# Optimization experiments

Hardware: AMD Instinct MI355X
Metric: run time of the kernel (lower is better)

Reference implementation:

```python
import jax, jax.numpy as jnp
import numpy as np

B, T, D, H = 4, 1024, 1024, 16


def setup_inputs() -> dict:
    key = jax.random.key(0)
    ks = jax.random.split(key, 7)
    x = jax.random.normal(ks[0], (B, T, D), dtype=jnp.float32)
    scale = 0.02
    Wq = jax.random.normal(ks[1], (D, D), dtype=jnp.float32) * scale
    Wk = jax.random.normal(ks[2], (D, D), dtype=jnp.float32) * scale
    Wv = jax.random.normal(ks[3], (D, D), dtype=jnp.float32) * scale
    bq = jax.random.normal(ks[4], (D,), dtype=jnp.float32) * scale
    bk = jax.random.normal(ks[5], (D,), dtype=jnp.float32) * scale
    bv = jax.random.normal(ks[6], (D,), dtype=jnp.float32) * scale
    temperature = jnp.ones((H, 1, 1), dtype=jnp.float32)  # nn.Parameter(torch.ones(H,1,1))
    return {"x": x, "Wq": Wq, "bq": bq, "Wk": Wk, "bk": bk, "Wv": Wv, "bv": bv,
            "temperature": temperature}


def reference(x, Wq, bq, Wk, bk, Wv, bv, temperature):
    b, t, d = x.shape
    h = temperature.shape[0]
    dh = d // h
    # torch: self.q(x).view(B, H, -1, T)  -- a RAW reshape of (B,T,D) -> (B,H,Dh,T)
    q = (x @ Wq + bq).reshape(b, h, dh, t)
    k = (x @ Wk + bk).reshape(b, h, dh, t)
    v = (x @ Wv + bv).reshape(b, h, dh, t)
    # attn = k^T @ v : (B,H,T,T), scaled per-head by temperature, softmax over last dim
    attn = jnp.einsum('bhdt,bhds->bhts', k, v) * temperature
    attn = jax.nn.softmax(attn, axis=-1)
    # out = q @ attn : (B,H,Dh,T), then RAW reshape back to (B,T,D)
    out = jnp.einsum('bhdt,bhts->bhds', q, attn)
    return out.reshape(b, t, d)
```

## Files before the change

### kernel.cpp

```cpp
#include <hip/hip_runtime.h>
#include <math.h>

#define Bv 4
#define Tv 1024
#define Dv 1024
#define Hv 16
#define DHv 64

typedef __attribute__((ext_vector_type(8))) short short8;
typedef __attribute__((ext_vector_type(4))) short short4v;
typedef __attribute__((ext_vector_type(4))) float f32x4;

#define MFMA16(a, b, c) __builtin_amdgcn_mfma_f32_16x16x32_bf16((a), (b), (c), 0, 0, 0)

__device__ __forceinline__ short f2bf(float f) {
    union { float f; unsigned u; } v; v.f = f;
    unsigned r = v.u + 0x7FFFu + ((v.u >> 16) & 1u);
    return (short)(r >> 16);
}

__device__ __forceinline__ void async16(const void* g, void* l) {
    __builtin_amdgcn_global_load_lds(
        (const __attribute__((address_space(1))) void*)g,
        (__attribute__((address_space(3))) void*)l, 16, 0, 0);
}

__device__ __forceinline__ short8 frag64(const short* buf, int r, int cw) {
    return *(const short8*)&buf[r * 64 + ((cw ^ (r & 7)) << 3)];
}

__device__ __forceinline__ short8 frag32(const short* buf, int r, int cw) {
    return *(const short8*)&buf[r * 32 + (((cw ^ r) & 3) << 3)];
}

__global__ __launch_bounds__(256) void cast_x(const float* __restrict__ x, short* __restrict__ xb) {
    const int idx = blockIdx.x * 256 + threadIdx.x;
    float4 v = ((const float4*)x)[idx];
    short4v o;
    o[0] = f2bf(v.x); o[1] = f2bf(v.y); o[2] = f2bf(v.z); o[3] = f2bf(v.w);
    ((short4v*)xb)[idx] = o;
}

__global__ __launch_bounds__(256) void w_cast_t(
    const float* __restrict__ Wq, const float* __restrict__ Wk, const float* __restrict__ Wv,
    short* __restrict__ Wt)
{
    const float* W = (blockIdx.z == 0) ? Wq : (blockIdx.z == 1) ? Wk : Wv;
    short* Wto = Wt + (size_t)blockIdx.z * 1048576;
    __shared__ short Tl[64 * 72];
    const int k0 = blockIdx.y * 64, n0 = blockIdx.x * 64;
    const int tid = threadIdx.x;
    {
        const int r = tid >> 2, c16 = (tid & 3) * 16;
        const float* src = W + (size_t)(k0 + r) * Dv + n0 + c16;
        float4 f0 = ((const float4*)src)[0], f1 = ((const float4*)src)[1];
        float4 f2 = ((const float4*)src)[2], f3 = ((const float4*)src)[3];
        short8 s0, s1;
        s0[0] = f2bf(f0.x); s0[1] = f2bf(f0.y); s0[2] = f2bf(f0.z); s0[3] = f2bf(f0.w);
        s0[4] = f2bf(f1.x); s0[5] = f2bf(f1.y); s0[6] = f2bf(f1.z); s0[7] = f2bf(f1.w);
        s1[0] = f2bf(f2.x); s1[1] = f2bf(f2.y); s1[2] = f2bf(f2.z); s1[3] = f2bf(f2.w);
        s1[4] = f2bf(f3.x); s1[5] = f2bf(f3.y); s1[6] = f2bf(f3.z); s1[7] = f2bf(f3.w);
        *(short8*)&Tl[r * 72 + c16] = s0;
        *(short8*)&Tl[r * 72 + c16 + 8] = s1;
    }
    __syncthreads();
#pragma unroll
    for (int p = 0; p < 2; p++) {
        const int n = p * 32 + (tid >> 3), j8 = (tid & 7) * 8;
        short8 o;
#pragma unroll
        for (int jj = 0; jj < 8; jj++) o[jj] = Tl[(j8 + jj) * 72 + n];
        *(short8*)&Wto[(size_t)(n0 + n) * Dv + k0 + j8] = o;
    }
}

__device__ __forceinline__ void stage_tile(
    const short* __restrict__ xb, const short* __restrict__ Wt,
    const int* aOff, const int* bOff, const int* dOff,
    short* smem, int sl, int k)
{
#pragma unroll
    for (int p = 0; p < 2; p++) {
        async16(xb + aOff[p] + k, smem + sl + dOff[p]);
        async16(Wt + bOff[p] + k, smem + 24576 + sl + dOff[p]);
    }
}

__device__ __forceinline__ void compute_tile(
    const short* smem, int sl, int RM, int CN, int c, int q, f32x4 acc[8][4])
{
    const short* Ac = smem + sl;
    const short* Bc = smem + 24576 + sl;
    short8 bf[4], af[8];
#pragma unroll
    for (int j = 0; j < 4; j++) bf[j] = frag32(Bc, CN + j * 16 + c, q);
#pragma unroll
    for (int m = 0; m < 8; m++) af[m] = frag32(Ac, RM + m * 16 + c, q);
    __builtin_amdgcn_s_setprio(1);
#pragma unroll
    for (int m = 0; m < 8; m++)
#pragma unroll
        for (int j = 0; j < 4; j++)
            acc[m][j] = MFMA16(af[m], bf[j], acc[m][j]);
    __builtin_amdgcn_s_setprio(0);
}

__global__ __launch_bounds__(512, 2) void qkv_mfma(
    const short* __restrict__ xb, const short* __restrict__ Wt3,
    const float* __restrict__ bq, const float* __restrict__ bk, const float* __restrict__ bv,
    short* __restrict__ Qo, short* __restrict__ Kt, short* __restrict__ Vt)
{
    const int z = blockIdx.z;
    const short* Wt = Wt3 + (size_t)z * 1048576;
    const float* bias = (z == 0) ? bq : (z == 1) ? bk : bv;

    __shared__ short smem[49152];

    const int tid = threadIdx.x;
    const int lane = tid & 63, w = tid >> 6;
    const int q = lane >> 4, c = lane & 15;
    const int wr = w >> 2, wc = w & 3;
    const int RM = wr * 128, CN = wc * 64;
    const int bm = blockIdx.y * 256, bn = blockIdx.x * 256;

    int aOff[2], bOff[2], dOff[2];
#pragma unroll
    for (int p = 0; p < 2; p++) {
        const int idx = p * 512 + tid;
        const int r = idx >> 2, cs = idx & 3, cg = (cs ^ r) & 3;
        aOff[p] = (bm + r) * Dv + cg * 8;
        bOff[p] = (bn + r) * Dv + cg * 8;
        dOff[p] = idx * 8;
    }

    f32x4 acc[8][4] = {};

    stage_tile(xb, Wt, aOff, bOff, dOff, smem, 0, 0);
    stage_tile(xb, Wt, aOff, bOff, dOff, smem, 8192, 32);

    int slC = 0, slS = 16384;
#pragma unroll 1
    for (int i = 0; i < 30; i++) {
        asm volatile("s_waitcnt vmcnt(4)" ::: "memory");
        __builtin_amdgcn_s_barrier();
        __builtin_amdgcn_sched_barrier(0);
        stage_tile(xb, Wt, aOff, bOff, dOff, smem, slS, (i + 2) * 32);
        compute_tile(smem, slC, RM, CN, c, q, acc);
        slC += 8192; if (slC == 24576) slC = 0;
        slS += 8192; if (slS == 24576) slS = 0;
    }
    asm volatile("s_waitcnt vmcnt(4)" ::: "memory");
    __builtin_amdgcn_s_barrier();
    __builtin_amdgcn_sched_barrier(0);
    compute_tile(smem, slC, RM, CN, c, q, acc);
    slC += 8192; if (slC == 24576) slC = 0;
    asm volatile("s_waitcnt vmcnt(0)" ::: "memory");
    __builtin_amdgcn_s_barrier();
    __builtin_amdgcn_sched_barrier(0);
    compute_tile(smem, slC, RM, CN, c, q, acc);

    if (z == 0) {
#pragma unroll
        for (int j = 0; j < 4; j++) {
            const int col = bn + CN + j * 16 + c;
            const float bb = bias[col];
#pragma unroll
            for (int m = 0; m < 8; m++) {
#pragma unroll
                for (int r = 0; r < 4; r++) {
                    const int row = bm + RM + m * 16 + q * 4 + r;
                    Qo[(size_t)row * Dv + col] = f2bf(acc[m][j][r] + bb);
                }
            }
        }
    } else {
        short* dst = (z == 1) ? Kt : Vt;
        short* T = smem;
        const int hb = bm >> 6;
#pragma unroll
        for (int nh = 0; nh < 2; nh++) {
            __syncthreads();
            if ((wc >> 1) == nh) {
#pragma unroll
                for (int j = 0; j < 4; j++) {
                    const int nl = (wc & 1) * 64 + j * 16 + c;
                    const float bb = bias[bn + nh * 128 + nl];
#pragma unroll
                    for (int m = 0; m < 8; m++) {
                        short4v pk;
#pragma unroll
                        for (int r = 0; r < 4; r++) pk[r] = f2bf(acc[m][j][r] + bb);
                        *(short4v*)&T[nl * 264 + RM + m * 16 + q * 4] = pk;
                    }
                }
            }
            __syncthreads();
#pragma unroll
            for (int p = 0; p < 8; p++) {
                const int idx = p * 512 + tid;
                const int n = idx >> 5, k2 = idx & 31;
                short8 v = *(const short8*)&T[n * 264 + k2 * 8];
                const size_t addr = (size_t)(hb + (k2 >> 3)) * 65536 +
                                    (size_t)(bn + nh * 128 + n) * 64 + (k2 & 7) * 8;
                *(short8*)&dst[addr] = v;
            }
        }
    }
}

__global__ __launch_bounds__(256) void attn_stats(
    const short* __restrict__ Kt, const short* __restrict__ Vt,
    const float* __restrict__ temp,
    float* __restrict__ mOut, float* __restrict__ zOut)
{
    const int b = blockIdx.z, h = blockIdx.y, t0 = blockIdx.x * 64;
    const int bh = b * Hv + h;
    const float ts = temp[h];
    __shared__ short Ks[64 * 64];
    __shared__ short Vs[128 * 64];
    const int tid = threadIdx.x;
    const int lane = tid & 63, w = tid >> 6;
    const int q = lane >> 4, c = lane & 15;
    const short* Kbase = Kt + (size_t)bh * 65536;
    const short* Vbase = Vt + (size_t)bh * 65536;

#pragma unroll
    for (int p = 0; p < 2; p++) {
        const int idx = p * 256 + tid;
        const int r = idx >> 3, cs = idx & 7, cg = cs ^ (r & 7);
        async16(Kbase + (size_t)(t0 + r) * 64 + cg * 8, Ks + idx * 8);
    }

    float m_run[4], z_run[4];
#pragma unroll
    for (int r = 0; r < 4; r++) { m_run[r] = -INFINITY; z_run[r] = 0.f; }

    short8 aK0, aK1;
    for (int s0 = 0; s0 < Tv; s0 += 128) {
        __syncthreads();
#pragma unroll
        for (int p = 0; p < 4; p++) {
            const int idx = p * 256 + tid;
            const int r = idx >> 3, cs = idx & 7, cg = cs ^ (r & 7);
            async16(Vbase + (size_t)(s0 + r) * 64 + cg * 8, Vs + idx * 8);
        }
        __syncthreads();
        if (s0 == 0) {
            aK0 = frag64(Ks, w * 16 + c, q);
            aK1 = frag64(Ks, w * 16 + c, 4 + q);
        }
        float lv[8][4];
#pragma unroll
        for (int sf = 0; sf < 8; sf++) {
            short8 b0 = frag64(Vs, sf * 16 + c, q);
            short8 b1 = frag64(Vs, sf * 16 + c, 4 + q);
            f32x4 l = {0.f, 0.f, 0.f, 0.f};
            l = MFMA16(aK0, b0, l);
            l = MFMA16(aK1, b1, l);
#pragma unroll
            for (int r = 0; r < 4; r++) lv[sf][r] = l[r] * ts;
        }
#pragma unroll
        for (int r = 0; r < 4; r++) {
            float vmax = lv[0][r];
#pragma unroll
            for (int sf = 1; sf < 8; sf++) vmax = fmaxf(vmax, lv[sf][r]);
            float mn = fmaxf(m_run[r], vmax);
            float za = 0.f;
#pragma unroll
            for (int sf = 0; sf < 8; sf++) za += __expf(lv[sf][r] - mn);
            z_run[r] = z_run[r] * __expf(m_run[r] - mn) + za;
            m_run[r] = mn;
        }
    }
#pragma unroll
    for (int mask = 1; mask <= 8; mask <<= 1) {
#pragma unroll
        for (int r = 0; r < 4; r++) {
            float om = __shfl_xor(m_run[r], mask, 64);
            float oz = __shfl_xor(z_run[r], mask, 64);
            float mn = fmaxf(m_run[r], om);
            z_run[r] = z_run[r] * __expf(m_run[r] - mn) + oz * __expf(om - mn);
            m_run[r] = mn;
        }
    }
    if (c == 0) {
#pragma unroll
        for (int r = 0; r < 4; r++) {
            const int t = t0 + w * 16 + q * 4 + r;
            mOut[(size_t)bh * Tv + t] = m_run[r];
            zOut[(size_t)bh * Tv + t] = 1.f / z_run[r];
        }
    }
}

__global__ __launch_bounds__(256) void attn_out(
    const short* __restrict__ Qb, const short* __restrict__ Kt, const short* __restrict__ Vt,
    const float* __restrict__ temp, const float* __restrict__ mIn, const float* __restrict__ zIn,
    float* __restrict__ out)
{
    const int b = blockIdx.z, h = blockIdx.y, s0 = blockIdx.x * 128;
    const int bh = b * Hv + h;
    const float ts = temp[h];
    __shared__ short Vs[128 * 64];
    __shared__ short Ks[64 * 64];
    __shared__ short Qs[64 * 64];
    __shared__ short Pt[128 * 72];
    __shared__ float ms[64], zs[64];
    const int tid = threadIdx.x;
    const int lane = tid & 63, w = tid >> 6;
    const int q = lane >> 4, c = lane & 15;
    const short* Vbase = Vt + (size_t)bh * 65536;
    const short* Kbase = Kt + (size_t)bh * 65536;
    const short* Qbase = Qb + (size_t)(b * Tv + h * DHv) * Dv;

#pragma unroll
    for (int p = 0; p < 4; p++) {
        const int idx = p * 256 + tid;
        const int r = idx >> 3, cs = idx & 7, cg = cs ^ (r & 7);
        async16(Vbase + (size_t)(s0 + r) * 64 + cg * 8, Vs + idx * 8);
    }

    f32x4 acc[8] = {};

    for (int t0 = 0; t0 < Tv; t0 += 64) {
        __syncthreads();
#pragma unroll
        for (int p = 0; p < 2; p++) {
            const int idx = p * 256 + tid;
            const int r = idx >> 3, cs = idx & 7, cg = cs ^ (r & 7);
            async16(Kbase + (size_t)(t0 + r) * 64 + cg * 8, Ks + idx * 8);
            async16(Qbase + (size_t)r * Dv + t0 + cg * 8, Qs + idx * 8);
        }
        if (tid < 64) {
            ms[tid] = mIn[(size_t)bh * Tv + t0 + tid];
            zs[tid] = zIn[(size_t)bh * Tv + t0 + tid];
        }
        __syncthreads();

        short8 aK0 = frag64(Ks, w * 16 + c, q);
        short8 aK1 = frag64(Ks, w * 16 + c, 4 + q);
#pragma unroll
        for (int sf = 0; sf < 8; sf++) {
            short8 b0 = frag64(Vs, sf * 16 + c, q);
            short8 b1 = frag64(Vs, sf * 16 + c, 4 + q);
            f32x4 l = {0.f, 0.f, 0.f, 0.f};
            l = MFMA16(aK0, b0, l);
            l = MFMA16(aK1, b1, l);
            short4v p4;
#pragma unroll
            for (int r = 0; r < 4; r++) {
                const int tr = w * 16 + q * 4 + r;
                float p = __expf(l[r] * ts - ms[tr]) * zs[tr];
                p4[r] = f2bf(p);
            }
            *(short4v*)&Pt[(sf * 16 + c) * 72 + w * 16 + q * 4] = p4;
        }
        __syncthreads();

        short8 aQ0 = frag64(Qs, w * 16 + c, q);
        short8 aQ1 = frag64(Qs, w * 16 + c, 4 + q);
#pragma unroll
        for (int sf = 0; sf < 8; sf++) {
            short8 p0 = *(const short8*)&Pt[(sf * 16 + c) * 72 + q * 8];
            short8 p1 = *(const short8*)&Pt[(sf * 16 + c) * 72 + 32 + q * 8];
            acc[sf] = MFMA16(aQ0, p0, acc[sf]);
            acc[sf] = MFMA16(aQ1, p1, acc[sf]);
        }
    }

#pragma unroll
    for (int sf = 0; sf < 8; sf++) {
#pragma unroll
        for (int r = 0; r < 4; r++) {
            const int d = w * 16 + q * 4 + r;
            out[(size_t)(b * Tv + h * DHv + d) * Dv + s0 + sf * 16 + c] = acc[sf][r];
        }
    }
}

extern "C" void kernel_launch(void* const* d_in, const int* in_sizes, int n_in,
                              void* d_out, int out_size, void* d_ws, size_t ws_size,
                              hipStream_t stream) {
    const float* x    = (const float*)d_in[0];
    const float* Wq   = (const float*)d_in[1];
    const float* bq   = (const float*)d_in[2];
    const float* Wk   = (const float*)d_in[3];
    const float* bk   = (const float*)d_in[4];
    const float* Wv   = (const float*)d_in[5];
    const float* bv   = (const float*)d_in[6];
    const float* temp = (const float*)d_in[7];
    float* out = (float*)d_out;

    char* ws = (char*)d_ws;
    short* xb = (short*)(ws);
    short* Wt = (short*)(ws + ((size_t)8 << 20));
    short* Qb = (short*)(ws + ((size_t)14 << 20));
    short* Kt = (short*)(ws + ((size_t)22 << 20));
    short* Vt = (short*)(ws + ((size_t)30 << 20));
    float* mbuf = (float*)(ws + ((size_t)38 << 20));
    float* zbuf = mbuf + 65536;

    cast_x<<<4096, 256, 0, stream>>>(x, xb);
    w_cast_t<<<dim3(16, 16, 3), 256, 0, stream>>>(Wq, Wk, Wv, Wt);
    qkv_mfma<<<dim3(4, 16, 3), 512, 0, stream>>>(xb, Wt, bq, bk, bv, Qb, Kt, Vt);
    attn_stats<<<dim3(16, 16, 4), 256, 0, stream>>>(Kt, Vt, temp, mbuf, zbuf);
    attn_out<<<dim3(8, 16, 4), 256, 0, stream>>>(Qb, Kt, Vt, temp, mbuf, zbuf, out);
}
```

Baseline: 188.0 us.

## Double-buffer K/Q and V tiles in attention kernels, keep V fragments in registers

Both attention kernels now prefetch the next K/Q or V tile into a second LDS buffer while the current tile is computed. This removes one barrier per iteration and hides global load latency. attn_out holds the V fragments in registers, reuses the V region for the swizzled P tile, and loads all m/z statistics up front with async copies. Blocks are remapped so neighbouring workgroups share bh, and launch bounds plus s_setprio are added around the MFMA sections. The extra registers and LDS may lower occupancy, and the manual lgkmcnt barrier has to be ordered correctly.

```diff
diff --git a/kernel.cpp b/kernel.cpp
--- a/kernel.cpp
+++ b/kernel.cpp
@@ -31,6 +31,13 @@
 
 __device__ __forceinline__ short8 frag32(const short* buf, int r, int cw) {
     return *(const short8*)&buf[r * 32 + (((cw ^ r) & 3) << 3)];
+}
+
+__device__ __forceinline__ void lds_barrier() {
+    asm volatile("s_waitcnt lgkmcnt(0)" ::: "memory");
+    __builtin_amdgcn_sched_barrier(0);
+    __builtin_amdgcn_s_barrier();
+    __builtin_amdgcn_sched_barrier(0);
 }
 
 __global__ __launch_bounds__(256) void cast_x(const float* __restrict__ x, short* __restrict__ xb) {
@@ -208,58 +215,71 @@
     }
 }
 
-__global__ __launch_bounds__(256) void attn_stats(
+__global__ __launch_bounds__(256, 4) void attn_stats(
     const short* __restrict__ Kt, const short* __restrict__ Vt,
     const float* __restrict__ temp,
     float* __restrict__ mOut, float* __restrict__ zOut)
 {
-    const int b = blockIdx.z, h = blockIdx.y, t0 = blockIdx.x * 64;
-    const int bh = b * Hv + h;
-    const float ts = temp[h];
+    const int L = blockIdx.x + 16 * (blockIdx.y + 16 * blockIdx.z);
+    const int bh = (L & 7) + 8 * (L >> 7);
+    const int t0 = ((L >> 3) & 15) * 64;
+    const float ts = temp[bh & 15];
     __shared__ short Ks[64 * 64];
-    __shared__ short Vs[128 * 64];
+    __shared__ short Vs[2][128 * 64];
     const int tid = threadIdx.x;
     const int lane = tid & 63, w = tid >> 6;
     const int q = lane >> 4, c = lane & 15;
     const short* Kbase = Kt + (size_t)bh * 65536;
     const short* Vbase = Vt + (size_t)bh * 65536;
 
+    int vOff[4], vDst[4];
+#pragma unroll
+    for (int p = 0; p < 4; p++) {
+        const int idx = p * 256 + tid;
+        const int r = idx >> 3, cs = idx & 7, cg = cs ^ (r & 7);
+        vOff[p] = r * 64 + cg * 8;
+        vDst[p] = idx * 8;
+    }
 #pragma unroll
     for (int p = 0; p < 2; p++) {
         const int idx = p * 256 + tid;
         const int r = idx >> 3, cs = idx & 7, cg = cs ^ (r & 7);
         async16(Kbase + (size_t)(t0 + r) * 64 + cg * 8, Ks + idx * 8);
     }
+#pragma unroll
+    for (int p = 0; p < 4; p++) async16(Vbase + vOff[p], &Vs[0][0] + vDst[p]);
 
     float m_run[4], z_run[4];
 #pragma unroll
     for (int r = 0; r < 4; r++) { m_run[r] = -INFINITY; z_run[r] = 0.f; }
 
     short8 aK0, aK1;
-    for (int s0 = 0; s0 < Tv; s0 += 128) {
+#pragma unroll 1
+    for (int i = 0; i < 8; i++) {
         __syncthreads();
-#pragma unroll
-        for (int p = 0; p < 4; p++) {
-            const int idx = p * 256 + tid;
-            const int r = idx >> 3, cs = idx & 7, cg = cs ^ (r & 7);
-            async16(Vbase + (size_t)(s0 + r) * 64 + cg * 8, Vs + idx * 8);
-        }
-        __syncthreads();
-        if (s0 == 0) {
+        if (i < 7) {
+            const short* src = Vbase + (i + 1) * 8192;
+#pragma unroll
+            for (int p = 0; p < 4; p++) async16(src + vOff[p], &Vs[(i + 1) & 1][0] + vDst[p]);
+        }
+        if (i == 0) {
             aK0 = frag64(Ks, w * 16 + c, q);
             aK1 = frag64(Ks, w * 16 + c, 4 + q);
         }
+        const short* Vc = &Vs[i & 1][0];
         float lv[8][4];
+        __builtin_amdgcn_s_setprio(1);
 #pragma unroll
         for (int sf = 0; sf < 8; sf++) {
-            short8 b0 = frag64(Vs, sf * 16 + c, q);
-            short8 b1 = frag64(Vs, sf * 16 + c, 4 + q);
+            short8 b0 = frag64(Vc, sf * 16 + c, q);
+            short8 b1 = frag64(Vc, sf * 16 + c, 4 + q);
             f32x4 l = {0.f, 0.f, 0.f, 0.f};
             l = MFMA16(aK0, b0, l);
             l = MFMA16(aK1, b1, l);
 #pragma unroll
             for (int r = 0; r < 4; r++) lv[sf][r] = l[r] * ts;
         }
+        __builtin_amdgcn_s_setprio(0);
 #pragma unroll
         for (int r = 0; r < 4; r++) {
             float vmax = lv[0][r];
@@ -294,19 +314,21 @@
     }
 }
 
-__global__ __launch_bounds__(256) void attn_out(
+__global__ __launch_bounds__(256, 2) void attn_out(
     const short* __restrict__ Qb, const short* __restrict__ Kt, const short* __restrict__ Vt,
     const float* __restrict__ temp, const float* __restrict__ mIn, const float* __restrict__ zIn,
     float* __restrict__ out)
 {
-    const int b = blockIdx.z, h = blockIdx.y, s0 = blockIdx.x * 128;
-    const int bh = b * Hv + h;
+    const int L = blockIdx.x + 8 * (blockIdx.y + 16 * blockIdx.z);
+    const int bh = (L & 7) + 8 * (L >> 6);
+    const int s0 = ((L >> 3) & 7) * 128;
+    const int b = bh >> 4, h = bh & 15;
     const float ts = temp[h];
-    __shared__ short Vs[128 * 64];
-    __shared__ short Ks[64 * 64];
-    __shared__ short Qs[64 * 64];
-    __shared__ short Pt[128 * 72];
-    __shared__ float ms[64], zs[64];
+
+    __shared__ short smem[28672];
+    short* VsPt = smem;
+    float* msz = (float*)(smem + 24576);
+
     const int tid = threadIdx.x;
     const int lane = tid & 63, w = tid >> 6;
     const int q = lane >> 4, c = lane & 15;
@@ -314,59 +336,86 @@
     const short* Kbase = Kt + (size_t)bh * 65536;
     const short* Qbase = Qb + (size_t)(b * Tv + h * DHv) * Dv;
 
+    int kOff[2], qOff[2], dK[2], dQ[2];
+#pragma unroll
+    for (int p = 0; p < 2; p++) {
+        const int idx = p * 256 + tid;
+        const int r = idx >> 3, cs = idx & 7, cg = cs ^ (r & 7);
+        kOff[p] = r * 64 + cg * 8;
+        qOff[p] = r * 1024 + cg * 8;
+        dK[p] = idx * 8;
+        dQ[p] = 4096 + idx * 8;
+    }
+
 #pragma unroll
     for (int p = 0; p < 4; p++) {
         const int idx = p * 256 + tid;
         const int r = idx >> 3, cs = idx & 7, cg = cs ^ (r & 7);
-        async16(Vbase + (size_t)(s0 + r) * 64 + cg * 8, Vs + idx * 8);
+        async16(Vbase + (size_t)(s0 + r) * 64 + cg * 8, VsPt + idx * 8);
+    }
+    async16(mIn + (size_t)bh * Tv + tid * 4, (short*)msz + tid * 8);
+    async16(zIn + (size_t)bh * Tv + tid * 4, (short*)(msz + 1024) + tid * 8);
+#pragma unroll
+    for (int p = 0; p < 2; p++) {
+        async16(Kbase + kOff[p], smem + 8192 + dK[p]);
+        async16(Qbase + qOff[p], smem + 8192 + dQ[p]);
+    }
+    __syncthreads();
+
+    short8 vb0[8], vb1[8];
+#pragma unroll
+    for (int sf = 0; sf < 8; sf++) {
+        vb0[sf] = frag64(VsPt, sf * 16 + c, q);
+        vb1[sf] = frag64(VsPt, sf * 16 + c, 4 + q);
     }
 
     f32x4 acc[8] = {};
-
-    for (int t0 = 0; t0 < Tv; t0 += 64) {
+    short* Pt = VsPt;
+
+#pragma unroll 1
+    for (int i = 0; i < 16; i++) {
+        const short* kq = smem + 8192 + (i & 1) * 8192;
         __syncthreads();
-#pragma unroll
-        for (int p = 0; p < 2; p++) {
-            const int idx = p * 256 + tid;
-            const int r = idx >> 3, cs = idx & 7, cg = cs ^ (r & 7);
-            async16(Kbase + (size_t)(t0 + r) * 64 + cg * 8, Ks + idx * 8);
-            async16(Qbase + (size_t)r * Dv + t0 + cg * 8, Qs + idx * 8);
-        }
-        if (tid < 64) {
-            ms[tid] = mIn[(size_t)bh * Tv + t0 + tid];
-            zs[tid] = zIn[(size_t)bh * Tv + t0 + tid];
-        }
-        __syncthreads();
-
-        short8 aK0 = frag64(Ks, w * 16 + c, q);
-        short8 aK1 = frag64(Ks, w * 16 + c, 4 + q);
+        if (i < 15) {
+            short* nxt = smem + 8192 + ((i + 1) & 1) * 8192;
+            const int t1 = (i + 1) * 64;
+#pragma unroll
+            for (int p = 0; p < 2; p++) {
+                async16(Kbase + t1 * 64 + kOff[p], nxt + dK[p]);
+                async16(Qbase + t1 + qOff[p], nxt + dQ[p]);
+            }
+        }
+        short8 aK0 = frag64(kq, w * 16 + c, q);
+        short8 aK1 = frag64(kq, w * 16 + c, 4 + q);
+        const int tr0 = i * 64 + w * 16 + q * 4;
+        const float4 mv = *(const float4*)&msz[tr0];
+        const float4 zv = *(const float4*)&msz[1024 + tr0];
 #pragma unroll
         for (int sf = 0; sf < 8; sf++) {
-            short8 b0 = frag64(Vs, sf * 16 + c, q);
-            short8 b1 = frag64(Vs, sf * 16 + c, 4 + q);
             f32x4 l = {0.f, 0.f, 0.f, 0.f};
-            l = MFMA16(aK0, b0, l);
-            l = MFMA16(aK1, b1, l);
+            l = MFMA16(aK0, vb0[sf], l);
+            l = MFMA16(aK1, vb1[sf], l);
+            const int rr = sf * 16 + c;
             short4v p4;
-#pragma unroll
-            for (int r = 0; r < 4; r++) {
-                const int tr = w * 16 + q * 4 + r;
-                float p = __expf(l[r] * ts - ms[tr]) * zs[tr];
-                p4[r] = f2bf(p);
-            }
-            *(short4v*)&Pt[(sf * 16 + c) * 72 + w * 16 + q * 4] = p4;
-        }
-        __syncthreads();
-
+            p4[0] = f2bf(__expf(l[0] * ts - mv.x) * zv.x);
+            p4[1] = f2bf(__expf(l[1] * ts - mv.y) * zv.y);
+            p4[2] = f2bf(__expf(l[2] * ts - mv.z) * zv.z);
+            p4[3] = f2bf(__expf(l[3] * ts - mv.w) * zv.w);
+            *(short4v*)&Pt[rr * 64 + (((w * 2 + (q >> 1)) ^ (rr & 7)) << 3) + (q & 1) * 4] = p4;
+        }
+        lds_barrier();
+        const short* Qs = kq + 4096;
         short8 aQ0 = frag64(Qs, w * 16 + c, q);
         short8 aQ1 = frag64(Qs, w * 16 + c, 4 + q);
+        __builtin_amdgcn_s_setprio(1);
 #pragma unroll
         for (int sf = 0; sf < 8; sf++) {
-            short8 p0 = *(const short8*)&Pt[(sf * 16 + c) * 72 + q * 8];
-            short8 p1 = *(const short8*)&Pt[(sf * 16 + c) * 72 + 32 + q * 8];
+            short8 p0 = frag64(Pt, sf * 16 + c, q);
+            short8 p1 = frag64(Pt, sf * 16 + c, 4 + q);
             acc[sf] = MFMA16(aQ0, p0, acc[sf]);
             acc[sf] = MFMA16(aQ1, p1, acc[sf]);
         }
+        __builtin_amdgcn_s_setprio(0);
     }
 
 #pragma unroll
```

Result: faster. 176.9 us (-5.9%).
